# Kernel optimization log

Measured on AMD Instinct MI355X. Metric: run time of the kernel, lower is better.

The kernel has to match this reference:

```python
import jax, jax.numpy as jnp
import numpy as np

B = 128
K = 16
# (in_ch, featdim, dim) per stage, matching conv1..conv11
DIMS = [(3, 8, 2048), (8, 32, 1024), (32, 64, 512), (64, 64, 256), (64, 64, 128),
        (64, 128, 64), (128, 256, 32), (256, 512, 16), (512, 512, 8), (512, 512, 4),
        (512, 1024, 2)]


def setup_inputs() -> dict:
    key = jax.random.key(0)
    ks = jax.random.split(key, 64)
    inp = {"x": jax.random.normal(ks[0], (B, 3, 2048), dtype=jnp.float32)}
    i = 1
    for li, (cin, cf, d) in enumerate(DIMS, start=1):
        inp[f"W{li}"] = jax.random.normal(ks[i], (3 * cf, cin), dtype=jnp.float32) / np.sqrt(cin).astype(np.float32); i += 1
        inp[f"b{li}"] = jax.random.normal(ks[i], (3 * cf,), dtype=jnp.float32) * 0.01; i += 1
        inp[f"sel{li}"] = jax.random.randint(ks[i], (d,), 0, 3); i += 1
    inp["fcW"] = jax.random.normal(ks[i], (K, 1024), dtype=jnp.float32) / np.sqrt(1024).astype(np.float32); i += 1
    inp["fcb"] = jax.random.normal(ks[i], (K,), dtype=jnp.float32) * 0.01
    return inp


def kdconv(x, W, b, sel, featdim, dim):
    # 1x1 conv == per-position matmul: x [B, Cin, dim] -> y [B, 3*featdim, dim]
    y = jax.nn.relu(jnp.einsum('oi,bin->bon', W, x) + b[None, :, None])
    y = y.reshape(-1, featdim, 3, dim)
    # kd split-dim gather: pick one of the 3 feature groups per position
    y = jnp.take_along_axis(y, sel[None, None, None, :], axis=2)[:, :, 0, :]  # [B, featdim, dim]
    # pairwise max-pool of sibling leaves
    return y.reshape(-1, featdim, dim // 2, 2).max(axis=-1)  # [B, featdim, dim//2]


def reference(x, sel1, sel2, sel3, sel4, sel5, sel6, sel7, sel8, sel9, sel10, sel11,
              W1, b1, W2, b2, W3, b3, W4, b4, W5, b5, W6, b6, W7, b7, W8, b8,
              W9, b9, W10, b10, W11, b11, fcW, fcb):
    Ws = [W1, W2, W3, W4, W5, W6, W7, W8, W9, W10, W11]
    bs = [b1, b2, b3, b4, b5, b6, b7, b8, b9, b10, b11]
    sels = [sel1, sel2, sel3, sel4, sel5, sel6, sel7, sel8, sel9, sel10, sel11]
    h = x
    for (cin, cf, d), W, b, s in zip(DIMS, Ws, bs, sels):
        h = kdconv(h, W, b, s, cf, d)
    h = h.reshape(-1, 1024)  # [B, 1024]
    return jax.nn.log_softmax(h @ fcW.T + fcb, axis=-1)
```

## Files before the change

### kernel.cpp

```cpp
#include <hip/hip_runtime.h>
#include <math.h>

typedef __attribute__((ext_vector_type(8))) short bf16x8;
typedef __attribute__((ext_vector_type(4))) float f32x4;

__device__ __forceinline__ unsigned short f2bf(float f) {
    unsigned u = __builtin_bit_cast(unsigned, f);
    u += 0x7FFF + ((u >> 16) & 1);
    return (unsigned short)(u >> 16);
}
__device__ __forceinline__ float bf2f(unsigned short h) {
    unsigned u = ((unsigned)h) << 16;
    return __builtin_bit_cast(float, u);
}

#define O_W8 153600
#define O_W9 546816
#define O_W10 1333248
#define O_W11 2119680

template<int CIN>
__device__ __forceinline__ void mfma_tile(
    const unsigned short* a0, const unsigned short* a1,
    const unsigned short* b0p, const unsigned short* b1p,
    f32x4& acc0, f32x4& acc1)
{
#pragma unroll
    for (int k = 0; k < CIN; k += 32) {
        bf16x8 A0 = __builtin_bit_cast(bf16x8, *(const float4*)(const void*)(a0 + k));
        bf16x8 A1 = __builtin_bit_cast(bf16x8, *(const float4*)(const void*)(a1 + k));
        bf16x8 B0 = __builtin_bit_cast(bf16x8, *(const float4*)(const void*)(b0p + k));
        bf16x8 B1 = __builtin_bit_cast(bf16x8, *(const float4*)(const void*)(b1p + k));
        acc0 = __builtin_amdgcn_mfma_f32_16x16x32_bf16(A0, B0, acc0, 0, 0, 0);
        acc1 = __builtin_amdgcn_mfma_f32_16x16x32_bf16(A1, B1, acc1, 0, 0, 0);
    }
}

__device__ __forceinline__ void epilogue_store(
    unsigned short* dst, const f32x4& acc0, const f32x4& acc1,
    const float* bias, int fbase, int s0, int s1)
{
    unsigned short o[4];
#pragma unroll
    for (int r = 0; r < 4; ++r) {
        float v = fmaxf(fmaxf(acc0[r] + bias[(fbase + r) * 3 + s0],
                              acc1[r] + bias[(fbase + r) * 3 + s1]), 0.f);
        o[r] = f2bf(v);
    }
    *(ushort4*)dst = make_ushort4(o[0], o[1], o[2], o[3]);
}

__device__ __forceinline__ bf16x8 cvt8(const float* p) {
    float4 u0 = *(const float4*)p;
    float4 u1 = *(const float4*)(p + 4);
    bf16x8 r;
    r[0] = (short)f2bf(u0.x); r[1] = (short)f2bf(u0.y);
    r[2] = (short)f2bf(u0.z); r[3] = (short)f2bf(u0.w);
    r[4] = (short)f2bf(u1.x); r[5] = (short)f2bf(u1.y);
    r[6] = (short)f2bf(u1.z); r[7] = (short)f2bf(u1.w);
    return r;
}

struct FusedParams {
    const float* x;
    const float* W1; const float* B1; const int* S1;
    const float* W2; const float* B2; const int* S2;
    const float* Wsrc[9];
    const float* Bl[9];
    const int*   Sl[9];
    unsigned short* Wb;
    unsigned short* X8;
};

#define A_XS   0
#define A_L1O  25344
#define A_WSM  41728
#define A_L2O  45568
#define A_WB3  0
#define A_L3O  86528
#define A_WB4  45568
#define A_L4O  0
#define A_WB5  18432
#define A_L5O  46080
#define A_WB6  55296
#define A_L6O  0
#define ARENA_BYTES 123392

__global__ __launch_bounds__(512) void fused17_kernel(FusedParams P)
{
    const int tid = threadIdx.x;

    if (blockIdx.x >= 128) {
        int gt = (blockIdx.x - 128) * 512 + tid;
        const int we[4] = {393216, 786432, 786432, 1572864};
        const int wo[4] = {O_W8, O_W9, O_W10, O_W11};
#pragma unroll
        for (int li = 0; li < 4; ++li) {
            const float4* src = (const float4*)P.Wsrc[5 + li];
            ushort4* dst = (ushort4*)(P.Wb + wo[li]);
            int n4 = we[li] >> 2;
            for (int i = gt; i < n4; i += 32768) {
                float4 w = src[i];
                dst[i] = make_ushort4(f2bf(w.x), f2bf(w.y), f2bf(w.z), f2bf(w.w));
            }
        }
        return;
    }

    __shared__ __align__(16) char arena[ARENA_BYTES];

    const int bg   = blockIdx.x >> 4;
    const int sl   = blockIdx.x & 15;
    const int lane = tid & 63;
    const int wv   = tid >> 6;
    const int c    = lane & 15, q = lane >> 4;

    {
        float* xsf = (float*)(arena + A_XS);
        const float* xg = P.x + (size_t)(bg * 16) * 6144 + sl * 128;
        for (int i = tid; i < 6144; i += 512) {
            int b = i / 384;
            int r = i - b * 384;
            int cc = r >> 7, p = r & 127;
            xsf[b * 396 + cc * 132 + p] = xg[(size_t)b * 6144 + cc * 2048 + p];
        }
        float* wsm = (float*)(arena + A_WSM);
        for (int i = tid; i < 960; i += 512) {
            float v;
            if (i < 72)       v = P.W1[i];
            else if (i < 96)  v = P.B1[i - 72];
            else if (i < 864) v = P.W2[i - 96];
            else              v = P.B2[i - 864];
            wsm[i] = v;
        }
    }
    __syncthreads();

    {
        const float* xsf = (const float*)(arena + A_XS);
        const float* wl1 = (const float*)(arena + A_WSM);
        const float* bl1 = wl1 + 72;
        unsigned short* L1o = (unsigned short*)(arena + A_L1O);
        for (int i = tid; i < 1024; i += 512) {
            int n = i >> 4, b = i & 15;
            int np1 = sl * 64 + n;
            int s0 = P.S1[2 * np1], s1 = P.S1[2 * np1 + 1];
            const float* xb0 = xsf + b * 396 + 2 * n;
            float c0x = xb0[0],   c0y = xb0[1];
            float c1x = xb0[132], c1y = xb0[133];
            float c2x = xb0[264], c2y = xb0[265];
            unsigned short o[8];
#pragma unroll
            for (int f = 0; f < 8; ++f) {
                int r0 = f * 3 + s0, r1 = f * 3 + s1;
                float z0 = fmaf(wl1[r0*3+2], c2x, fmaf(wl1[r0*3+1], c1x, fmaf(wl1[r0*3+0], c0x, bl1[r0])));
                float z1 = fmaf(wl1[r1*3+2], c2y, fmaf(wl1[r1*3+1], c1y, fmaf(wl1[r1*3+0], c0y, bl1[r1])));
                o[f] = f2bf(fmaxf(fmaxf(z0, z1), 0.f));
            }
            unsigned short* dst = L1o + (n * 16 + b) * 8;
            *(ushort4*)dst       = make_ushort4(o[0], o[1], o[2], o[3]);
            *(ushort4*)(dst + 4) = make_ushort4(o[4], o[5], o[6], o[7]);
        }
    }
    __syncthreads();

    {
        const float* wl2 = (const float*)(arena + A_WSM) + 96;
        const float* bl2 = (const float*)(arena + A_WSM) + 864;
        const unsigned short* L1o = (const unsigned short*)(arena + A_L1O);
        unsigned short* L2o = (unsigned short*)(arena + A_L2O);
        {
            int i = tid;
            int n = i >> 4, b = i & 15;
            int np2 = sl * 32 + n;
            int s0 = P.S2[2 * np2], s1 = P.S2[2 * np2 + 1];
            const unsigned short* r0 = L1o + ((2 * n) * 16 + b) * 8;
            const unsigned short* r1 = L1o + ((2 * n + 1) * 16 + b) * 8;
            float xa[8], xb2[8];
            {
                ushort4 u0 = *(const ushort4*)r0, u1 = *(const ushort4*)(r0 + 4);
                ushort4 v0 = *(const ushort4*)r1, v1 = *(const ushort4*)(r1 + 4);
                xa[0]=bf2f(u0.x); xa[1]=bf2f(u0.y); xa[2]=bf2f(u0.z); xa[3]=bf2f(u0.w);
                xa[4]=bf2f(u1.x); xa[5]=bf2f(u1.y); xa[6]=bf2f(u1.z); xa[7]=bf2f(u1.w);
                xb2[0]=bf2f(v0.x); xb2[1]=bf2f(v0.y); xb2[2]=bf2f(v0.z); xb2[3]=bf2f(v0.w);
                xb2[4]=bf2f(v1.x); xb2[5]=bf2f(v1.y); xb2[6]=bf2f(v1.z); xb2[7]=bf2f(v1.w);
            }
            unsigned short o[32];
#pragma unroll
            for (int f = 0; f < 32; ++f) {
                const float* w0 = &wl2[(f * 3 + s0) * 8];
                const float* w1 = &wl2[(f * 3 + s1) * 8];
                float z0 = bl2[f * 3 + s0], z1 = bl2[f * 3 + s1];
#pragma unroll
                for (int k = 0; k < 8; ++k) {
                    z0 = fmaf(w0[k], xa[k], z0);
                    z1 = fmaf(w1[k], xb2[k], z1);
                }
                o[f] = f2bf(fmaxf(fmaxf(z0, z1), 0.f));
            }
            unsigned short* dst = L2o + (n * 16 + b) * 40;
#pragma unroll
            for (int i2 = 0; i2 < 8; ++i2)
                *(ushort4*)(dst + 4 * i2) = make_ushort4(o[4*i2], o[4*i2+1], o[4*i2+2], o[4*i2+3]);
        }
    }
    __syncthreads();

    {
        unsigned short* wb = (unsigned short*)(arena + A_WB3);
        const float* Wf = P.Wsrc[0];
        for (int i = tid; i < 6144; i += 512) {
            int row = i >> 5, k = i & 31;
            wb[row * 40 + k] = f2bf(Wf[i]);
        }
    }
    __syncthreads();

    {
        const unsigned short* wb  = (const unsigned short*)(arena + A_WB3);
        const unsigned short* L2o = (const unsigned short*)(arena + A_L2O);
        unsigned short* L3o = (unsigned short*)(arena + A_L3O);
        const int* S3 = P.Sl[0]; const float* B3 = P.Bl[0];
        for (int t = wv; t < 64; t += 8) {
            int n3 = t >> 2, ft = t & 3;
            int np = sl * 16 + n3;
            int s0 = __builtin_amdgcn_readfirstlane(S3[2 * np]);
            int s1 = __builtin_amdgcn_readfirstlane(S3[2 * np + 1]);
            int f0 = ft * 16;
            const unsigned short* a0 = wb + ((f0 + c) * 3 + s0) * 40 + q * 8;
            const unsigned short* a1 = wb + ((f0 + c) * 3 + s1) * 40 + q * 8;
            const unsigned short* bp0 = L2o + ((2 * n3) * 16 + c) * 40 + q * 8;
            const unsigned short* bp1 = L2o + ((2 * n3 + 1) * 16 + c) * 40 + q * 8;
            f32x4 acc0 = {0.f,0.f,0.f,0.f}, acc1 = {0.f,0.f,0.f,0.f};
            mfma_tile<32>(a0, a1, bp0, bp1, acc0, acc1);
            epilogue_store(L3o + (n3 * 16 + c) * 72 + f0 + q * 4,
                           acc0, acc1, B3, f0 + q * 4, s0, s1);
        }
    }
    __syncthreads();

    {
        unsigned short* wb = (unsigned short*)(arena + A_WB4);
        const float* Wf = P.Wsrc[1];
        for (int i = tid; i < 12288; i += 512) {
            int row = i >> 6, k = i & 63;
            wb[row * 72 + k] = f2bf(Wf[i]);
        }
    }
    __syncthreads();

    {
        const unsigned short* wb  = (const unsigned short*)(arena + A_WB4);
        const unsigned short* L3o = (const unsigned short*)(arena + A_L3O);
        unsigned short* L4o = (unsigned short*)(arena + A_L4O);
        const int* S4 = P.Sl[1]; const float* B4 = P.Bl[1];
        for (int t = wv; t < 32; t += 8) {
            int n4 = t >> 2, ft = t & 3;
            int np = sl * 8 + n4;
            int s0 = __builtin_amdgcn_readfirstlane(S4[2 * np]);
            int s1 = __builtin_amdgcn_readfirstlane(S4[2 * np + 1]);
            int f0 = ft * 16;
            const unsigned short* a0 = wb + ((f0 + c) * 3 + s0) * 72 + q * 8;
            const unsigned short* a1 = wb + ((f0 + c) * 3 + s1) * 72 + q * 8;
            const unsigned short* bp0 = L3o + ((2 * n4) * 16 + c) * 72 + q * 8;
            const unsigned short* bp1 = L3o + ((2 * n4 + 1) * 16 + c) * 72 + q * 8;
            f32x4 acc0 = {0.f,0.f,0.f,0.f}, acc1 = {0.f,0.f,0.f,0.f};
            mfma_tile<64>(a0, a1, bp0, bp1, acc0, acc1);
            epilogue_store(L4o + (n4 * 16 + c) * 72 + f0 + q * 4,
                           acc0, acc1, B4, f0 + q * 4, s0, s1);
        }
    }
    __syncthreads();

    {
        unsigned short* wb = (unsigned short*)(arena + A_WB5);
        const float* Wf = P.Wsrc[2];
        for (int i = tid; i < 12288; i += 512) {
            int row = i >> 6, k = i & 63;
            wb[row * 72 + k] = f2bf(Wf[i]);
        }
    }
    __syncthreads();

    {
        const unsigned short* wb  = (const unsigned short*)(arena + A_WB5);
        const unsigned short* L4o = (const unsigned short*)(arena + A_L4O);
        unsigned short* L5o = (unsigned short*)(arena + A_L5O);
        const int* S5 = P.Sl[2]; const float* B5 = P.Bl[2];
        for (int t = wv; t < 16; t += 8) {
            int n5 = t >> 2, ft = t & 3;
            int np = sl * 4 + n5;
            int s0 = __builtin_amdgcn_readfirstlane(S5[2 * np]);
            int s1 = __builtin_amdgcn_readfirstlane(S5[2 * np + 1]);
            int f0 = ft * 16;
            const unsigned short* a0 = wb + ((f0 + c) * 3 + s0) * 72 + q * 8;
            const unsigned short* a1 = wb + ((f0 + c) * 3 + s1) * 72 + q * 8;
            const unsigned short* bp0 = L4o + ((2 * n5) * 16 + c) * 72 + q * 8;
            const unsigned short* bp1 = L4o + ((2 * n5 + 1) * 16 + c) * 72 + q * 8;
            f32x4 acc0 = {0.f,0.f,0.f,0.f}, acc1 = {0.f,0.f,0.f,0.f};
            mfma_tile<64>(a0, a1, bp0, bp1, acc0, acc1);
            epilogue_store(L5o + (n5 * 16 + c) * 72 + f0 + q * 4,
                           acc0, acc1, B5, f0 + q * 4, s0, s1);
        }
    }
    __syncthreads();

    {
        unsigned short* wb = (unsigned short*)(arena + A_WB6);
        const float* Wf = P.Wsrc[3];
        for (int i = tid; i < 24576; i += 512) {
            int row = i >> 6, k = i & 63;
            wb[row * 72 + k] = f2bf(Wf[i]);
        }
    }
    __syncthreads();

    {
        const unsigned short* wb  = (const unsigned short*)(arena + A_WB6);
        const unsigned short* L5o = (const unsigned short*)(arena + A_L5O);
        unsigned short* L6o = (unsigned short*)(arena + A_L6O);
        const int* S6 = P.Sl[3]; const float* B6 = P.Bl[3];
        for (int t = wv; t < 16; t += 8) {
            int n6 = t >> 3, ft = t & 7;
            int np = sl * 2 + n6;
            int s0 = __builtin_amdgcn_readfirstlane(S6[2 * np]);
            int s1 = __builtin_amdgcn_readfirstlane(S6[2 * np + 1]);
            int f0 = ft * 16;
            const unsigned short* a0 = wb + ((f0 + c) * 3 + s0) * 72 + q * 8;
            const unsigned short* a1 = wb + ((f0 + c) * 3 + s1) * 72 + q * 8;
            const unsigned short* bp0 = L5o + ((2 * n6) * 16 + c) * 72 + q * 8;
            const unsigned short* bp1 = L5o + ((2 * n6 + 1) * 16 + c) * 72 + q * 8;
            f32x4 acc0 = {0.f,0.f,0.f,0.f}, acc1 = {0.f,0.f,0.f,0.f};
            mfma_tile<64>(a0, a1, bp0, bp1, acc0, acc1);
            epilogue_store(L6o + (n6 * 16 + c) * 136 + f0 + q * 4,
                           acc0, acc1, B6, f0 + q * 4, s0, s1);
        }
    }
    __syncthreads();

    {
        const unsigned short* L6o = (const unsigned short*)(arena + A_L6O);
        const float* W7f = P.Wsrc[4];
        const int* S7 = P.Sl[4]; const float* B7 = P.Bl[4];
        int s0 = __builtin_amdgcn_readfirstlane(S7[2 * sl]);
        int s1 = __builtin_amdgcn_readfirstlane(S7[2 * sl + 1]);
        for (int t = wv; t < 16; t += 8) {
            int f0 = t * 16;
            const float* wa0 = W7f + (size_t)((f0 + c) * 3 + s0) * 128;
            const float* wa1 = W7f + (size_t)((f0 + c) * 3 + s1) * 128;
            const unsigned short* bp0 = L6o + (0 * 16 + c) * 136;
            const unsigned short* bp1 = L6o + (1 * 16 + c) * 136;
            f32x4 acc0 = {0.f,0.f,0.f,0.f}, acc1 = {0.f,0.f,0.f,0.f};
#pragma unroll
            for (int k = 0; k < 128; k += 32) {
                bf16x8 A0 = cvt8(wa0 + k + q * 8);
                bf16x8 A1 = cvt8(wa1 + k + q * 8);
                bf16x8 B0 = __builtin_bit_cast(bf16x8, *(const float4*)(const void*)(bp0 + k + q * 8));
                bf16x8 B1 = __builtin_bit_cast(bf16x8, *(const float4*)(const void*)(bp1 + k + q * 8));
                acc0 = __builtin_amdgcn_mfma_f32_16x16x32_bf16(A0, B0, acc0, 0, 0, 0);
                acc1 = __builtin_amdgcn_mfma_f32_16x16x32_bf16(A1, B1, acc1, 0, 0, 0);
            }
            epilogue_store(P.X8 + ((size_t)sl * 128 + bg * 16 + c) * 256 + f0 + q * 4,
                           acc0, acc1, B7, f0 + q * 4, s0, s1);
        }
    }
}

template<int CIN, int CF, int NP, int MW, int NW>
__global__ __launch_bounds__(256) void mfma_kernel(
    const unsigned short* __restrict__ Xin,
    const unsigned short* __restrict__ Wb,
    const float* __restrict__ bias,
    const int*   __restrict__ sel,
    unsigned short* __restrict__ Xout)
{
    constexpr int FT = CF / (16 * MW);
    constexpr int BT = 128 / (16 * NW);

    const int wid  = threadIdx.x >> 6;
    const int lane = threadIdx.x & 63;
    const int task = blockIdx.x * 4 + wid;
    const int bi = task % BT;
    const int fi = (task / BT) % FT;
    const int n  = task / (BT * FT);

    const int c = lane & 15;
    const int q = lane >> 4;
    const int s0 = __builtin_amdgcn_readfirstlane(sel[2 * n]);
    const int s1 = __builtin_amdgcn_readfirstlane(sel[2 * n + 1]);

    const int f0 = fi * 16 * MW;
    const int b0 = bi * 16 * NW;

    const unsigned short* ap[2][MW];
    const unsigned short* bp[2][NW];
#pragma unroll
    for (int p = 0; p < 2; ++p) {
        int s = p ? s1 : s0;
#pragma unroll
        for (int mi = 0; mi < MW; ++mi)
            ap[p][mi] = Wb + (size_t)((f0 + mi * 16 + c) * 3 + s) * CIN + q * 8;
#pragma unroll
        for (int ni = 0; ni < NW; ++ni)
            bp[p][ni] = Xin + ((size_t)(2 * n + p) * 128 + b0 + ni * 16 + c) * CIN + q * 8;
    }

    f32x4 acc[2][MW][NW];
#pragma unroll
    for (int p = 0; p < 2; ++p)
#pragma unroll
        for (int mi = 0; mi < MW; ++mi)
#pragma unroll
            for (int ni = 0; ni < NW; ++ni)
                acc[p][mi][ni] = (f32x4){0.f, 0.f, 0.f, 0.f};

#pragma unroll 2
    for (int k = 0; k < CIN; k += 32) {
        bf16x8 A[2][MW], B[2][NW];
#pragma unroll
        for (int p = 0; p < 2; ++p) {
#pragma unroll
            for (int mi = 0; mi < MW; ++mi)
                A[p][mi] = __builtin_bit_cast(bf16x8, *(const float4*)(const void*)(ap[p][mi] + k));
#pragma unroll
            for (int ni = 0; ni < NW; ++ni)
                B[p][ni] = __builtin_bit_cast(bf16x8, *(const float4*)(const void*)(bp[p][ni] + k));
        }
#pragma unroll
        for (int p = 0; p < 2; ++p)
#pragma unroll
            for (int mi = 0; mi < MW; ++mi)
#pragma unroll
                for (int ni = 0; ni < NW; ++ni)
                    acc[p][mi][ni] = __builtin_amdgcn_mfma_f32_16x16x32_bf16(
                        A[p][mi], B[p][ni], acc[p][mi][ni], 0, 0, 0);
    }

#pragma unroll
    for (int mi = 0; mi < MW; ++mi) {
        int fbase = f0 + mi * 16 + q * 4;
#pragma unroll
        for (int ni = 0; ni < NW; ++ni) {
            int b = b0 + ni * 16 + c;
            epilogue_store(Xout + ((size_t)n * 128 + b) * CF + fbase,
                           acc[0][mi][ni], acc[1][mi][ni], bias, fbase, s0, s1);
        }
    }
}

__global__ __launch_bounds__(256) void fc_logsoftmax_kernel(
    const unsigned short* __restrict__ h, const float* __restrict__ fcW,
    const float* __restrict__ fcb, float* __restrict__ out)
{
    int b   = blockIdx.x;
    int tid = threadIdx.x;
    int k     = tid & 15;
    int chunk = tid >> 4;

    const float* __restrict__ wk = fcW + (size_t)k * 1024;
    const unsigned short* hb = h + (size_t)b * 1024;

    float partial = 0.0f;
    int j0 = chunk * 64;
#pragma unroll 8
    for (int j = 0; j < 64; ++j)
        partial = fmaf(bf2f(hb[j0 + j]), wk[j0 + j], partial);

    __shared__ float red[16][17];
    red[chunk][k] = partial;
    __syncthreads();

    __shared__ float logits[16];
    if (tid < 16) {
        float s = fcb[tid];
#pragma unroll
        for (int c = 0; c < 16; ++c) s += red[c][tid];
        logits[tid] = s;
    }
    __syncthreads();

    if (tid < 16) {
        float mx = -INFINITY;
#pragma unroll
        for (int kk = 0; kk < 16; ++kk) mx = fmaxf(mx, logits[kk]);
        float se = 0.0f;
#pragma unroll
        for (int kk = 0; kk < 16; ++kk) se += expf(logits[kk] - mx);
        out[b * 16 + tid] = logits[tid] - mx - logf(se);
    }
}

extern "C" void kernel_launch(void* const* d_in, const int* in_sizes, int n_in,
                              void* d_out, int out_size, void* d_ws, size_t ws_size,
                              hipStream_t stream)
{
#define WL(i) (const float*)d_in[1 + 3 * (i)]
#define BL(i) (const float*)d_in[2 + 3 * (i)]
#define SL(i) (const int*)  d_in[3 + 3 * (i)]

    unsigned short* bufA = (unsigned short*)d_ws;
    unsigned short* bufB = bufA + 2u * 1024u * 1024u;
    unsigned short* Wb   = bufB + 2u * 1024u * 1024u;

    FusedParams FP;
    FP.x  = (const float*)d_in[0];
    FP.W1 = WL(0); FP.B1 = BL(0); FP.S1 = SL(0);
    FP.W2 = WL(1); FP.B2 = BL(1); FP.S2 = SL(1);
    for (int i = 0; i < 9; ++i) {
        FP.Wsrc[i] = WL(2 + i);
        FP.Bl[i]   = BL(2 + i);
        FP.Sl[i]   = SL(2 + i);
    }
    FP.Wb = Wb; FP.X8 = bufA;
    fused17_kernel<<<192, 512, 0, stream>>>(FP);

    mfma_kernel<256, 512, 8, 2, 2><<<128, 256, 0, stream>>>(bufA, Wb + O_W8,  BL(7),  SL(7),  bufB);
    mfma_kernel<512, 512, 4, 1, 1><<<256, 256, 0, stream>>>(bufB, Wb + O_W9,  BL(8),  SL(8),  bufA);
    mfma_kernel<512, 512, 2, 1, 1><<<128, 256, 0, stream>>>(bufA, Wb + O_W10, BL(9),  SL(9),  bufB);
    mfma_kernel<512, 1024, 1, 1, 1><<<128, 256, 0, stream>>>(bufB, Wb + O_W11, BL(10), SL(10), bufA);

    fc_logsoftmax_kernel<<<128, 256, 0, stream>>>(bufA, (const float*)d_in[34], (const float*)d_in[35], (float*)d_out);

#undef WL
#undef BL
#undef SL
}
```

Measured before the change: 208.7 us.

## Pre-pack all weights to bf16 in a separate kernel; read layers 3-7 weights from global

Adds a dedicated pack kernel that converts the weights of layers 3-11 to bf16 in global memory before the fused kernel runs. The fused kernel no longer converts each layer's weights into shared memory per block or runs extra packing blocks. Layers 3-7 now read bf16 weights directly from global/L2, which removes the per-block conversion passes and their syncs and shrinks the LDS arena. The cost is an extra kernel launch, a serial dependency on the pack kernel, and unpadded global weight reads in the MFMA loops in place of LDS reads.

```diff
diff --git a/kernel.cpp b/kernel.cpp
--- a/kernel.cpp
+++ b/kernel.cpp
@@ -14,6 +14,11 @@
     return __builtin_bit_cast(float, u);
 }
 
+#define O_W3 0
+#define O_W4 6144
+#define O_W5 18432
+#define O_W6 30720
+#define O_W7 55296
 #define O_W8 153600
 #define O_W9 546816
 #define O_W10 1333248
@@ -50,25 +55,33 @@
     *(ushort4*)dst = make_ushort4(o[0], o[1], o[2], o[3]);
 }
 
-__device__ __forceinline__ bf16x8 cvt8(const float* p) {
-    float4 u0 = *(const float4*)p;
-    float4 u1 = *(const float4*)(p + 4);
-    bf16x8 r;
-    r[0] = (short)f2bf(u0.x); r[1] = (short)f2bf(u0.y);
-    r[2] = (short)f2bf(u0.z); r[3] = (short)f2bf(u0.w);
-    r[4] = (short)f2bf(u1.x); r[5] = (short)f2bf(u1.y);
-    r[6] = (short)f2bf(u1.z); r[7] = (short)f2bf(u1.w);
-    return r;
+struct PackParams { const float* Wsrc[9]; unsigned short* Wb; };
+
+__global__ __launch_bounds__(256) void pack_w_kernel(PackParams P)
+{
+    int gt = blockIdx.x * 256 + threadIdx.x;
+    const int we[9] = {6144, 12288, 12288, 24576, 98304, 393216, 786432, 786432, 1572864};
+    int off = 0;
+#pragma unroll
+    for (int li = 0; li < 9; ++li) {
+        const float4* src = (const float4*)P.Wsrc[li];
+        ushort4* dst = (ushort4*)(P.Wb + off);
+        int n4 = we[li] >> 2;
+        for (int i = gt; i < n4; i += 65536) {
+            float4 w = src[i];
+            dst[i] = make_ushort4(f2bf(w.x), f2bf(w.y), f2bf(w.z), f2bf(w.w));
+        }
+        off += we[li];
+    }
 }
 
 struct FusedParams {
     const float* x;
     const float* W1; const float* B1; const int* S1;
     const float* W2; const float* B2; const int* S2;
-    const float* Wsrc[9];
     const float* Bl[9];
     const int*   Sl[9];
-    unsigned short* Wb;
+    const unsigned short* Wb;
     unsigned short* X8;
 };
 
@@ -76,44 +89,28 @@
 #define A_L1O  25344
 #define A_WSM  41728
 #define A_L2O  45568
-#define A_WB3  0
-#define A_L3O  86528
-#define A_WB4  45568
-#define A_L4O  0
-#define A_WB5  18432
-#define A_L5O  46080
-#define A_WB6  55296
-#define A_L6O  0
-#define ARENA_BYTES 123392
+#define A_L3O  0
+#define A_L4O  45568
+#define A_L5O  0
+#define A_L6O  45568
+#define ARENA_BYTES 86528
 
 __global__ __launch_bounds__(512) void fused17_kernel(FusedParams P)
 {
-    const int tid = threadIdx.x;
-
-    if (blockIdx.x >= 128) {
-        int gt = (blockIdx.x - 128) * 512 + tid;
-        const int we[4] = {393216, 786432, 786432, 1572864};
-        const int wo[4] = {O_W8, O_W9, O_W10, O_W11};
-#pragma unroll
-        for (int li = 0; li < 4; ++li) {
-            const float4* src = (const float4*)P.Wsrc[5 + li];
-            ushort4* dst = (ushort4*)(P.Wb + wo[li]);
-            int n4 = we[li] >> 2;
-            for (int i = gt; i < n4; i += 32768) {
-                float4 w = src[i];
-                dst[i] = make_ushort4(f2bf(w.x), f2bf(w.y), f2bf(w.z), f2bf(w.w));
-            }
-        }
-        return;
-    }
-
     __shared__ __align__(16) char arena[ARENA_BYTES];
 
+    const int tid  = threadIdx.x;
     const int bg   = blockIdx.x >> 4;
     const int sl   = blockIdx.x & 15;
     const int lane = tid & 63;
     const int wv   = tid >> 6;
     const int c    = lane & 15, q = lane >> 4;
+
+    const unsigned short* W3b = P.Wb + O_W3;
+    const unsigned short* W4b = P.Wb + O_W4;
+    const unsigned short* W5b = P.Wb + O_W5;
+    const unsigned short* W6b = P.Wb + O_W6;
+    const unsigned short* W7b = P.Wb + O_W7;
 
     {
         float* xsf = (float*)(arena + A_XS);
@@ -207,28 +204,18 @@
     __syncthreads();
 
     {
-        unsigned short* wb = (unsigned short*)(arena + A_WB3);
-        const float* Wf = P.Wsrc[0];
-        for (int i = tid; i < 6144; i += 512) {
-            int row = i >> 5, k = i & 31;
-            wb[row * 40 + k] = f2bf(Wf[i]);
-        }
-    }
-    __syncthreads();
-
-    {
-        const unsigned short* wb  = (const unsigned short*)(arena + A_WB3);
         const unsigned short* L2o = (const unsigned short*)(arena + A_L2O);
         unsigned short* L3o = (unsigned short*)(arena + A_L3O);
         const int* S3 = P.Sl[0]; const float* B3 = P.Bl[0];
+#pragma unroll 2
         for (int t = wv; t < 64; t += 8) {
             int n3 = t >> 2, ft = t & 3;
             int np = sl * 16 + n3;
             int s0 = __builtin_amdgcn_readfirstlane(S3[2 * np]);
             int s1 = __builtin_amdgcn_readfirstlane(S3[2 * np + 1]);
             int f0 = ft * 16;
-            const unsigned short* a0 = wb + ((f0 + c) * 3 + s0) * 40 + q * 8;
-            const unsigned short* a1 = wb + ((f0 + c) * 3 + s1) * 40 + q * 8;
+            const unsigned short* a0 = W3b + ((f0 + c) * 3 + s0) * 32 + q * 8;
+            const unsigned short* a1 = W3b + ((f0 + c) * 3 + s1) * 32 + q * 8;
             const unsigned short* bp0 = L2o + ((2 * n3) * 16 + c) * 40 + q * 8;
             const unsigned short* bp1 = L2o + ((2 * n3 + 1) * 16 + c) * 40 + q * 8;
             f32x4 acc0 = {0.f,0.f,0.f,0.f}, acc1 = {0.f,0.f,0.f,0.f};
@@ -240,28 +227,18 @@
     __syncthreads();
 
     {
-        unsigned short* wb = (unsigned short*)(arena + A_WB4);
-        const float* Wf = P.Wsrc[1];
-        for (int i = tid; i < 12288; i += 512) {
-            int row = i >> 6, k = i & 63;
-            wb[row * 72 + k] = f2bf(Wf[i]);
-        }
-    }
-    __syncthreads();
-
-    {
-        const unsigned short* wb  = (const unsigned short*)(arena + A_WB4);
         const unsigned short* L3o = (const unsigned short*)(arena + A_L3O);
         unsigned short* L4o = (unsigned short*)(arena + A_L4O);
         const int* S4 = P.Sl[1]; const float* B4 = P.Bl[1];
+#pragma unroll 2
         for (int t = wv; t < 32; t += 8) {
             int n4 = t >> 2, ft = t & 3;
             int np = sl * 8 + n4;
             int s0 = __builtin_amdgcn_readfirstlane(S4[2 * np]);
             int s1 = __builtin_amdgcn_readfirstlane(S4[2 * np + 1]);
             int f0 = ft * 16;
-            const unsigned short* a0 = wb + ((f0 + c) * 3 + s0) * 72 + q * 8;
-            const unsigned short* a1 = wb + ((f0 + c) * 3 + s1) * 72 + q * 8;
+            const unsigned short* a0 = W4b + ((f0 + c) * 3 + s0) * 64 + q * 8;
+            const unsigned short* a1 = W4b + ((f0 + c) * 3 + s1) * 64 + q * 8;
             const unsigned short* bp0 = L3o + ((2 * n4) * 16 + c) * 72 + q * 8;
             const unsigned short* bp1 = L3o + ((2 * n4 + 1) * 16 + c) * 72 + q * 8;
             f32x4 acc0 = {0.f,0.f,0.f,0.f}, acc1 = {0.f,0.f,0.f,0.f};
@@ -273,17 +250,6 @@
     __syncthreads();
 
     {
-        unsigned short* wb = (unsigned short*)(arena + A_WB5);
-        const float* Wf = P.Wsrc[2];
-        for (int i = tid; i < 12288; i += 512) {
-            int row = i >> 6, k = i & 63;
-            wb[row * 72 + k] = f2bf(Wf[i]);
-        }
-    }
-    __syncthreads();
-
-    {
-        const unsigned short* wb  = (const unsigned short*)(arena + A_WB5);
         const unsigned short* L4o = (const unsigned short*)(arena + A_L4O);
         unsigned short* L5o = (unsigned short*)(arena + A_L5O);
         const int* S5 = P.Sl[2]; const float* B5 = P.Bl[2];
@@ -293,8 +259,8 @@
             int s0 = __builtin_amdgcn_readfirstlane(S5[2 * np]);
             int s1 = __builtin_amdgcn_readfirstlane(S5[2 * np + 1]);
             int f0 = ft * 16;
-            const unsigned short* a0 = wb + ((f0 + c) * 3 + s0) * 72 + q * 8;
-            const unsigned short* a1 = wb + ((f0 + c) * 3 + s1) * 72 + q * 8;
+            const unsigned short* a0 = W5b + ((f0 + c) * 3 + s0) * 64 + q * 8;
+            const unsigned short* a1 = W5b + ((f0 + c) * 3 + s1) * 64 + q * 8;
             const unsigned short* bp0 = L4o + ((2 * n5) * 16 + c) * 72 + q * 8;
             const unsigned short* bp1 = L4o + ((2 * n5 + 1) * 16 + c) * 72 + q * 8;
             f32x4 acc0 = {0.f,0.f,0.f,0.f}, acc1 = {0.f,0.f,0.f,0.f};
@@ -306,17 +272,6 @@
     __syncthreads();
 
     {
-        unsigned short* wb = (unsigned short*)(arena + A_WB6);
-        const float* Wf = P.Wsrc[3];
-        for (int i = tid; i < 24576; i += 512) {
-            int row = i >> 6, k = i & 63;
-            wb[row * 72 + k] = f2bf(Wf[i]);
-        }
-    }
-    __syncthreads();
-
-    {
-        const unsigned short* wb  = (const unsigned short*)(arena + A_WB6);
         const unsigned short* L5o = (const unsigned short*)(arena + A_L5O);
         unsigned short* L6o = (unsigned short*)(arena + A_L6O);
         const int* S6 = P.Sl[3]; const float* B6 = P.Bl[3];
@@ -326,8 +281,8 @@
             int s0 = __builtin_amdgcn_readfirstlane(S6[2 * np]);
             int s1 = __builtin_amdgcn_readfirstlane(S6[2 * np + 1]);
             int f0 = ft * 16;
-            const unsigned short* a0 = wb + ((f0 + c) * 3 + s0) * 72 + q * 8;
-            const unsigned short* a1 = wb + ((f0 + c) * 3 + s1) * 72 + q * 8;
+            const unsigned short* a0 = W6b + ((f0 + c) * 3 + s0) * 64 + q * 8;
+            const unsigned short* a1 = W6b + ((f0 + c) * 3 + s1) * 64 + q * 8;
             const unsigned short* bp0 = L5o + ((2 * n6) * 16 + c) * 72 + q * 8;
             const unsigned short* bp1 = L5o + ((2 * n6 + 1) * 16 + c) * 72 + q * 8;
             f32x4 acc0 = {0.f,0.f,0.f,0.f}, acc1 = {0.f,0.f,0.f,0.f};
@@ -340,26 +295,18 @@
 
     {
         const unsigned short* L6o = (const unsigned short*)(arena + A_L6O);
-        const float* W7f = P.Wsrc[4];
         const int* S7 = P.Sl[4]; const float* B7 = P.Bl[4];
         int s0 = __builtin_amdgcn_readfirstlane(S7[2 * sl]);
         int s1 = __builtin_amdgcn_readfirstlane(S7[2 * sl + 1]);
+#pragma unroll 2
         for (int t = wv; t < 16; t += 8) {
             int f0 = t * 16;
-            const float* wa0 = W7f + (size_t)((f0 + c) * 3 + s0) * 128;
-            const float* wa1 = W7f + (size_t)((f0 + c) * 3 + s1) * 128;
-            const unsigned short* bp0 = L6o + (0 * 16 + c) * 136;
-            const unsigned short* bp1 = L6o + (1 * 16 + c) * 136;
+            const unsigned short* a0 = W7b + (size_t)((f0 + c) * 3 + s0) * 128 + q * 8;
+            const unsigned short* a1 = W7b + (size_t)((f0 + c) * 3 + s1) * 128 + q * 8;
+            const unsigned short* bp0 = L6o + (0 * 16 + c) * 136 + q * 8;
+            const unsigned short* bp1 = L6o + (1 * 16 + c) * 136 + q * 8;
             f32x4 acc0 = {0.f,0.f,0.f,0.f}, acc1 = {0.f,0.f,0.f,0.f};
-#pragma unroll
-            for (int k = 0; k < 128; k += 32) {
-                bf16x8 A0 = cvt8(wa0 + k + q * 8);
-                bf16x8 A1 = cvt8(wa1 + k + q * 8);
-                bf16x8 B0 = __builtin_bit_cast(bf16x8, *(const float4*)(const void*)(bp0 + k + q * 8));
-                bf16x8 B1 = __builtin_bit_cast(bf16x8, *(const float4*)(const void*)(bp1 + k + q * 8));
-                acc0 = __builtin_amdgcn_mfma_f32_16x16x32_bf16(A0, B0, acc0, 0, 0, 0);
-                acc1 = __builtin_amdgcn_mfma_f32_16x16x32_bf16(A1, B1, acc1, 0, 0, 0);
-            }
+            mfma_tile<128>(a0, a1, bp0, bp1, acc0, acc1);
             epilogue_store(P.X8 + ((size_t)sl * 128 + bg * 16 + c) * 256 + f0 + q * 4,
                            acc0, acc1, B7, f0 + q * 4, s0, s1);
         }
@@ -502,17 +449,21 @@
     unsigned short* bufB = bufA + 2u * 1024u * 1024u;
     unsigned short* Wb   = bufB + 2u * 1024u * 1024u;
 
+    PackParams PP;
+    for (int i = 0; i < 9; ++i) PP.Wsrc[i] = WL(2 + i);
+    PP.Wb = Wb;
+    pack_w_kernel<<<256, 256, 0, stream>>>(PP);
+
     FusedParams FP;
     FP.x  = (const float*)d_in[0];
     FP.W1 = WL(0); FP.B1 = BL(0); FP.S1 = SL(0);
     FP.W2 = WL(1); FP.B2 = BL(1); FP.S2 = SL(1);
     for (int i = 0; i < 9; ++i) {
-        FP.Wsrc[i] = WL(2 + i);
-        FP.Bl[i]   = BL(2 + i);
-        FP.Sl[i]   = SL(2 + i);
+        FP.Bl[i] = BL(2 + i);
+        FP.Sl[i] = SL(2 + i);
     }
     FP.Wb = Wb; FP.X8 = bufA;
-    fused17_kernel<<<192, 512, 0, stream>>>(FP);
+    fused17_kernel<<<128, 512, 0, stream>>>(FP);
 
     mfma_kernel<256, 512, 8, 2, 2><<<128, 256, 0, stream>>>(bufA, Wb + O_W8,  BL(7),  SL(7),  bufB);
     mfma_kernel<512, 512, 4, 1, 1><<<256, 256, 0, stream>>>(bufB, Wb + O_W9,  BL(8),  SL(8),  bufA);
```

Measured after the change: 211.6 us. No clear change (+1.4%).
